# Performance work log

Measured on AMD Instinct MI355X. Metric: run time of the kernel, lower is better.

Reference implementation:

```python
import jax, jax.numpy as jnp
import numpy as np

EPS = 1e-5

def _layer_norm(x, w, b):
    mu = jnp.mean(x, axis=-1, keepdims=True)
    var = jnp.var(x, axis=-1, keepdims=True)
    return (x - mu) * jax.lax.rsqrt(var + EPS) * w + b

def setup_inputs() -> dict:
    key = jax.random.key(0)
    ks = jax.random.split(key, 9)
    B, N, D, H = 1, 768, 128, 128
    s_in = 1.0 / np.sqrt(D)
    s_h = 1.0 / np.sqrt(H)
    return {
        "x": jax.random.normal(ks[0], (B, N, N, D), dtype=jnp.float32),
        "mask": jnp.ones((B, N, N), dtype=jnp.float32),
        "norm_w": jnp.ones((D,), dtype=jnp.float32),
        "norm_b": jnp.zeros((D,), dtype=jnp.float32),
        "w_left": jax.random.normal(ks[1], (H, D), dtype=jnp.float32) * s_in,
        "w_right": jax.random.normal(ks[2], (H, D), dtype=jnp.float32) * s_in,
        "w_left_gate": jax.random.normal(ks[3], (H, D), dtype=jnp.float32) * s_in,
        "w_right_gate": jax.random.normal(ks[4], (H, D), dtype=jnp.float32) * s_in,
        "w_out_gate": jax.random.normal(ks[5], (H, D), dtype=jnp.float32) * s_in,
        "out_norm_w": jnp.ones((H,), dtype=jnp.float32),
        "out_norm_b": jnp.zeros((H,), dtype=jnp.float32),
        "w_out": jax.random.normal(ks[6], (D, H), dtype=jnp.float32) * s_h,
    }

def reference(x, mask, norm_w, norm_b, w_left, w_right, w_left_gate,
              w_right_gate, w_out_gate, out_norm_w, out_norm_b, w_out):
    # x: [B, N, N, D], mask: [B, N, N]
    xn = _layer_norm(x, norm_w, norm_b)
    m = mask[..., None]  # [B, N, N, 1]
    left = (xn @ w_left.T) * m * jax.nn.sigmoid(xn @ w_left_gate.T)
    right = (xn @ w_right.T) * m * jax.nn.sigmoid(xn @ w_right_gate.T)
    out_gate = jax.nn.sigmoid(xn @ w_out_gate.T)
    # per-channel triangular matmul in bf16, as in the original
    out = jnp.einsum('bikd,bjkd->bijd',
                     left.astype(jnp.bfloat16),
                     right.astype(jnp.bfloat16)).astype(jnp.float32)
    out = _layer_norm(out, out_norm_w, out_norm_b) * out_gate
    return out @ w_out.T
```

## Files before the change

kernel.cpp:

```cpp
#include <hip/hip_runtime.h>

typedef unsigned short u16;
typedef unsigned int   u32;
typedef short short8 __attribute__((ext_vector_type(8)));
typedef _Float16 half8 __attribute__((ext_vector_type(8)));
typedef float f32x4  __attribute__((ext_vector_type(4)));

#define NN 768
#define N2 (768*768)

__device__ __forceinline__ u16 f2b(float f) {
  u32 u = __float_as_uint(f);
  return (u16)((u + 0x7FFFu + ((u >> 16) & 1u)) >> 16);
}
__device__ __forceinline__ float b2f(u16 h) { return __uint_as_float(((u32)h) << 16); }
__device__ __forceinline__ u16 f2h(float f) {
  _Float16 h = (_Float16)f;
  return __builtin_bit_cast(u16, h);
}
__device__ __forceinline__ float h2f(u16 h) { return (float)__builtin_bit_cast(_Float16, h); }

__device__ __forceinline__ void gl_lds16(const void* g, void* lds) {
  __builtin_amdgcn_global_load_lds((__attribute__((address_space(1))) void*)(void*)g,
                                   (__attribute__((address_space(3))) void*)lds, 16, 0, 0);
}

__device__ __forceinline__ short8 frag256(const u16* base, int row, int k) {
  int c = k >> 3;
  int slot = ((c & 7) ^ (row & 7)) | (c & 8);
  return *(const short8*)(base + row*128 + slot*8);
}
__device__ __forceinline__ short8 frag128(const u16* base, int row, int k) {
  int c = k >> 3;
  int slot = (c ^ row) & 7;
  return *(const short8*)(base + row*64 + slot*8);
}
__device__ __forceinline__ f32x4 mfma_bf(short8 a, short8 b, f32x4 c) {
  return __builtin_amdgcn_mfma_f32_16x16x32_bf16(a, b, c, 0, 0, 0);
}
__device__ __forceinline__ f32x4 mfma_h(short8 a, short8 b, f32x4 c) {
  return __builtin_amdgcn_mfma_f32_16x16x32_f16(
      __builtin_bit_cast(half8, a), __builtin_bit_cast(half8, b), c, 0, 0, 0);
}

__global__ void k0_cvt(const float* __restrict__ w0, const float* __restrict__ w1,
                       const float* __restrict__ w2, const float* __restrict__ w3,
                       const float* __restrict__ w4, const float* __restrict__ w5,
                       u16* __restrict__ dst) {
  int idx = blockIdx.x*256 + threadIdx.x;
  int m = idx >> 14, o = idx & 16383;
  const float* s;
  switch (m) { case 0: s=w0; break; case 1: s=w1; break; case 2: s=w2; break;
               case 3: s=w3; break; case 4: s=w4; break; default: s=w5; }
  dst[idx] = f2h(s[o]);
}

__global__ __launch_bounds__(256, 2) void k1_proj(
    const float* __restrict__ x, const float* __restrict__ mask,
    const float* __restrict__ nw, const float* __restrict__ nb,
    const u16* __restrict__ wbf,
    u16* __restrict__ left_t, u16* __restrict__ right_t, u16* __restrict__ gate_ws)
{
  __shared__ __align__(16) u16 As[128*128];
  __shared__ __align__(16) u16 Bs[128*128];
  __shared__ float maskL[128];

  const int tid = threadIdx.x, w = tid>>6, l = tid&63;
  const long r0 = (long)blockIdx.x * 128;

  if (tid < 128) maskL[tid] = mask[r0 + tid];

  {
    const int c0v = l*2;
    const float nw0 = nw[c0v], nw1 = nw[c0v+1], nb0 = nb[c0v], nb1 = nb[c0v+1];
    for (int m = 0; m < 32; ++m) {
      int row = w*32 + m;
      float2 v = *(const float2*)(x + (r0 + row)*128 + c0v);
      float s = v.x + v.y, s2 = v.x*v.x + v.y*v.y;
      #pragma unroll
      for (int off = 1; off < 64; off <<= 1) {
        s  += __shfl_xor(s,  off, 64);
        s2 += __shfl_xor(s2, off, 64);
      }
      float mu = s * 0.0078125f;
      float rs = rsqrtf(s2 * 0.0078125f - mu*mu + 1e-5f);
      u32 pk = (u32)f2h((v.x - mu)*rs*nw0 + nb0)
             | ((u32)f2h((v.y - mu)*rs*nw1 + nb1) << 16);
      int c = l >> 2, slot = ((c&7)^(row&7)) | (c&8);
      *(u32*)(As + row*128 + slot*8 + (l&3)*2) = pk;
    }
  }
  __syncthreads();

  const int q = l>>4, mm = l&15;

  auto stageB = [&](const u16* wb) {
    #pragma unroll
    for (int c2 = 0; c2 < 8; ++c2) {
      int chunk = c2*4 + w;
      int rowv = chunk*4 + (l>>4);
      int sl = l & 15;
      int g16 = ((sl&7)^(rowv&7)) | (sl&8);
      gl_lds16(wb + rowv*128 + g16*8, Bs + chunk*512);
    }
  };

  f32x4 accA[2][8], accB[2][8];
  auto mfmaInto = [&](f32x4 (&acc)[2][8]) {
    #pragma unroll
    for (int rt = 0; rt < 2; ++rt)
      #pragma unroll
      for (int ct = 0; ct < 8; ++ct) acc[rt][ct] = (f32x4){0.f,0.f,0.f,0.f};
    #pragma unroll
    for (int ks = 0; ks < 4; ++ks) {
      int k = ks*32 + q*8;
      short8 a0 = frag256(As, w*32 + mm, k);
      short8 a1 = frag256(As, w*32 + 16 + mm, k);
      #pragma unroll
      for (int ct = 0; ct < 8; ++ct) {
        short8 bv = frag256(Bs, ct*16 + mm, k);
        acc[0][ct] = mfma_h(a0, bv, acc[0][ct]);
        acc[1][ct] = mfma_h(a1, bv, acc[1][ct]);
      }
    }
  };

  auto sigmoidAll = [&](f32x4 (&acc)[2][8]) {
    #pragma unroll
    for (int rt = 0; rt < 2; ++rt)
      #pragma unroll
      for (int ct = 0; ct < 8; ++ct)
        #pragma unroll
        for (int r = 0; r < 4; ++r)
          acc[rt][ct][r] = 1.f/(1.f + __expf(-acc[rt][ct][r]));
  };

  auto combineMask = [&](f32x4 (&av)[2][8], f32x4 (&ag)[2][8]) {
    float mk[2][4];
    #pragma unroll
    for (int rt = 0; rt < 2; ++rt)
      #pragma unroll
      for (int r = 0; r < 4; ++r) mk[rt][r] = maskL[w*32 + rt*16 + q*4 + r];
    #pragma unroll
    for (int rt = 0; rt < 2; ++rt)
      #pragma unroll
      for (int ct = 0; ct < 8; ++ct)
        #pragma unroll
        for (int r = 0; r < 4; ++r)
          av[rt][ct][r] *= mk[rt][r] * ag[rt][ct][r];
  };

  auto transposeStore = [&](f32x4 (&av)[2][8], u16* dst) {
    #pragma unroll
    for (int rt = 0; rt < 2; ++rt) {
      #pragma unroll
      for (int ct = 0; ct < 8; ++ct) {
        int kl = w*32 + rt*16 + q*4;
        int d  = ct*16 + mm;
        int c = kl >> 3, slot = ((c&7)^(d&7)) | (c&8);
        u32 p0 = (u32)f2b(av[rt][ct][0]) | ((u32)f2b(av[rt][ct][1])<<16);
        u32 p1 = (u32)f2b(av[rt][ct][2]) | ((u32)f2b(av[rt][ct][3])<<16);
        *(uint2*)(Bs + d*128 + slot*8 + (kl&7)) = make_uint2(p0, p1);
      }
    }
    __syncthreads();
    #pragma unroll
    for (int g = 0; g < 2; ++g) {
      int d = w*32 + g*16 + (l>>2);
      #pragma unroll
      for (int p = 0; p < 4; ++p) {
        int cc = p*4 + (l&3);
        int slot = ((cc&7)^(d&7)) | (cc&8);
        uint4 vv = *(const uint4*)(Bs + d*128 + slot*8);
        *(uint4*)(dst + (long)d*N2 + r0 + cc*8) = vv;
      }
    }
    __syncthreads();
  };

  stageB(wbf + 0*16384); __syncthreads();
  mfmaInto(accA); sigmoidAll(accA);
  __syncthreads();
  stageB(wbf + 1*16384); __syncthreads();
  mfmaInto(accB); combineMask(accB, accA);
  __syncthreads();
  transposeStore(accB, left_t);
  stageB(wbf + 2*16384); __syncthreads();
  mfmaInto(accA); sigmoidAll(accA);
  __syncthreads();
  stageB(wbf + 3*16384); __syncthreads();
  mfmaInto(accB); combineMask(accB, accA);
  __syncthreads();
  transposeStore(accB, right_t);
  stageB(wbf + 4*16384); __syncthreads();
  mfmaInto(accA); sigmoidAll(accA);
  #pragma unroll
  for (int rt = 0; rt < 2; ++rt)
    #pragma unroll
    for (int ct = 0; ct < 8; ++ct)
      #pragma unroll
      for (int r = 0; r < 4; ++r) {
        int row = w*32 + rt*16 + q*4 + r, dd = ct*16 + mm;
        gate_ws[(r0 + row)*128 + dd] = f2h(accA[rt][ct][r]);
      }
}

__global__ __launch_bounds__(256, 2) void k2_gemm(
    const u16* __restrict__ left_t, const u16* __restrict__ right_t, u16* __restrict__ out_ws)
{
  __shared__ __align__(16) u16 As[128*64];
  __shared__ __align__(16) u16 Bs[128*64];
  const int tid = threadIdx.x, w = tid>>6, l = tid&63;
  int bid = blockIdx.x;
  int d = bid / 36, t36 = bid % 36;
  int it = t36 / 6, jt = t36 % 6;
  const u16* Lb = left_t  + (long)d*N2 + (long)it*128*NN;
  const u16* Rb = right_t + (long)d*N2 + (long)jt*128*NN;
  const int wi = w & 1, wj = w >> 1;
  const int q = l>>4, mm = l&15;
  const int rloc = l>>3, sv = l&7;
  f32x4 acc[4][4];
  #pragma unroll
  for (int a2 = 0; a2 < 4; ++a2)
    #pragma unroll
    for (int b2 = 0; b2 < 4; ++b2) acc[a2][b2] = (f32x4){0.f,0.f,0.f,0.f};

  for (int kt = 0; kt < 12; ++kt) {
    __syncthreads();
    int k0 = kt*64;
    #pragma unroll
    for (int c2 = 0; c2 < 4; ++c2) {
      int chunk = c2*4 + w;
      int row = chunk*8 + rloc;
      int g8 = sv ^ (row & 7);
      gl_lds16(Lb + row*NN + k0 + g8*8, As + chunk*512);
      gl_lds16(Rb + row*NN + k0 + g8*8, Bs + chunk*512);
    }
    __syncthreads();
    #pragma unroll
    for (int kk = 0; kk < 64; kk += 32) {
      int k = kk + q*8;
      short8 af[4], bf[4];
      #pragma unroll
      for (int a2 = 0; a2 < 4; ++a2) af[a2] = frag128(As, wi*64 + a2*16 + mm, k);
      #pragma unroll
      for (int b2 = 0; b2 < 4; ++b2) bf[b2] = frag128(Bs, wj*64 + b2*16 + mm, k);
      #pragma unroll
      for (int a2 = 0; a2 < 4; ++a2)
        #pragma unroll
        for (int b2 = 0; b2 < 4; ++b2)
          acc[a2][b2] = mfma_bf(af[a2], bf[b2], acc[a2][b2]);
    }
  }
  u16* Ob = out_ws + (long)d*N2 + (long)(it*128)*NN + jt*128;
  #pragma unroll
  for (int a2 = 0; a2 < 4; ++a2)
    #pragma unroll
    for (int b2 = 0; b2 < 4; ++b2)
      #pragma unroll
      for (int r = 0; r < 4; ++r)
        Ob[(long)(wi*64 + a2*16 + q*4 + r)*NN + wj*64 + b2*16 + mm] = f2b(acc[a2][b2][r]);
}

__global__ __launch_bounds__(256, 2) void k3_out(
    const u16* __restrict__ out_ws, const u16* __restrict__ gate_ws,
    const float* __restrict__ onw, const float* __restrict__ onb,
    const u16* __restrict__ wbo, float* __restrict__ out)
{
  __shared__ __align__(16) u16 As[64*128];
  __shared__ __align__(16) u16 Bs[128*128];
  __shared__ float P[8][64];
  const int tid = threadIdx.x, w = tid>>6, l = tid&63;
  const int i = blockIdx.y, jt = blockIdx.x;
  const long base = (long)i*NN + jt*64;

  float v[32]; float s = 0.f, s2 = 0.f;
  const u16* src = out_ws + base + l;
  #pragma unroll
  for (int dd = 0; dd < 32; ++dd) {
    float f = b2f(src[(long)(w*32 + dd)*N2]);
    v[dd] = f; s += f; s2 += f*f;
  }
  P[w][l] = s; P[4+w][l] = s2;
  #pragma unroll
  for (int c2 = 0; c2 < 8; ++c2) {
    int chunk = c2*4 + w;
    int rowv = chunk*4 + (l>>4);
    int sl = l&15;
    int g16 = ((sl&7)^(rowv&7)) | (sl&8);
    gl_lds16(wbo + rowv*128 + g16*8, Bs + chunk*512);
  }
  __syncthreads();
  float sum = P[0][l]+P[1][l]+P[2][l]+P[3][l];
  float sq  = P[4][l]+P[5][l]+P[6][l]+P[7][l];
  float mu = sum * 0.0078125f;
  float rs = rsqrtf(sq * 0.0078125f - mu*mu + 1e-5f);

  const u16* gp = gate_ws + (base + l)*128 + w*32;
  #pragma unroll
  for (int hh = 0; hh < 32; hh += 2) {
    int h = w*32 + hh;
    u32 gpr = *(const u32*)(gp + hh);
    float g0 = h2f((u16)gpr), g1 = h2f((u16)(gpr>>16));
    float a0 = ((v[hh]   - mu)*rs*onw[h]   + onb[h])   * g0;
    float a1 = ((v[hh+1] - mu)*rs*onw[h+1] + onb[h+1]) * g1;
    u32 pk = (u32)f2h(a0) | ((u32)f2h(a1)<<16);
    int c = h >> 3, slot = ((c&7)^(l&7)) | (c&8);
    *(u32*)(As + l*128 + slot*8 + (h&7)) = pk;
  }
  __syncthreads();

  const int q = l>>4, mm = l&15;
  f32x4 acc[8];
  #pragma unroll
  for (int b2 = 0; b2 < 8; ++b2) acc[b2] = (f32x4){0.f,0.f,0.f,0.f};
  #pragma unroll
  for (int ks = 0; ks < 4; ++ks) {
    int k = ks*32 + q*8;
    short8 af = frag256(As, w*16 + mm, k);
    #pragma unroll
    for (int b2 = 0; b2 < 8; ++b2)
      acc[b2] = mfma_h(af, frag256(Bs, b2*16 + mm, k), acc[b2]);
  }
  float* ob = out + (base + w*16)*128;
  #pragma unroll
  for (int b2 = 0; b2 < 8; ++b2)
    #pragma unroll
    for (int r = 0; r < 4; ++r)
      ob[(long)(q*4 + r)*128 + b2*16 + mm] = acc[b2][r];
}

extern "C" void kernel_launch(void* const* d_in, const int* in_sizes, int n_in,
                              void* d_out, int out_size, void* d_ws, size_t ws_size,
                              hipStream_t stream) {
  const float* x    = (const float*)d_in[0];
  const float* mask = (const float*)d_in[1];
  const float* nw   = (const float*)d_in[2];
  const float* nb   = (const float*)d_in[3];
  const float* wl   = (const float*)d_in[4];
  const float* wr   = (const float*)d_in[5];
  const float* wlg  = (const float*)d_in[6];
  const float* wrg  = (const float*)d_in[7];
  const float* wog  = (const float*)d_in[8];
  const float* onw  = (const float*)d_in[9];
  const float* onb  = (const float*)d_in[10];
  const float* wo   = (const float*)d_in[11];

  if (ws_size < (size_t)4*N2*128*2 + 6*16384*2) return;
  u16* left_t  = (u16*)d_ws;
  u16* right_t = left_t  + (size_t)N2*128;
  u16* gate_ws = right_t + (size_t)N2*128;
  u16* out_ws  = gate_ws + (size_t)N2*128;
  u16* wbf     = out_ws  + (size_t)N2*128;

  k0_cvt<<<384, 256, 0, stream>>>(wlg, wl, wrg, wr, wog, wo, wbf);
  k1_proj<<<4608, 256, 0, stream>>>(x, mask, nw, nb, wbf, left_t, right_t, gate_ws);
  k2_gemm<<<4608, 256, 0, stream>>>(left_t, right_t, out_ws);
  k3_out<<<dim3(12, 768), 256, 0, stream>>>(out_ws, gate_ws, onw, onb, wbf + 5*16384, (float*)d_out);
}
```

Before: 1.138 ms.

## Restructure projection kernel: global-fragment weights, fused gate pairs, transposed gate layout

```diff
diff --git a/kernel.cpp b/kernel.cpp
--- a/kernel.cpp
+++ b/kernel.cpp
@@ -35,34 +35,47 @@
   int slot = (c ^ row) & 7;
   return *(const short8*)(base + row*64 + slot*8);
 }
+__device__ __forceinline__ short8 fragG(const u16* wg, int row, int k) {
+  return *(const short8*)(wg + (((k >> 3)*128) + row)*8);
+}
 __device__ __forceinline__ f32x4 mfma_bf(short8 a, short8 b, f32x4 c) {
   return __builtin_amdgcn_mfma_f32_16x16x32_bf16(a, b, c, 0, 0, 0);
 }
 __device__ __forceinline__ f32x4 mfma_h(short8 a, short8 b, f32x4 c) {
   return __builtin_amdgcn_mfma_f32_16x16x32_f16(
       __builtin_bit_cast(half8, a), __builtin_bit_cast(half8, b), c, 0, 0, 0);
+}
+__device__ __forceinline__ float sigm(float x) {
+  return __builtin_amdgcn_rcpf(1.f + __expf(-x));
 }
 
 __global__ void k0_cvt(const float* __restrict__ w0, const float* __restrict__ w1,
                        const float* __restrict__ w2, const float* __restrict__ w3,
                        const float* __restrict__ w4, const float* __restrict__ w5,
                        u16* __restrict__ dst) {
-  int idx = blockIdx.x*256 + threadIdx.x;
-  int m = idx >> 14, o = idx & 16383;
+  int t = blockIdx.x*256 + threadIdx.x;
+  int m = t >> 11, o = t & 2047;
+  int h = o >> 4, c = o & 15;
   const float* s;
   switch (m) { case 0: s=w0; break; case 1: s=w1; break; case 2: s=w2; break;
                case 3: s=w3; break; case 4: s=w4; break; default: s=w5; }
-  dst[idx] = f2h(s[o]);
+  const float* p = s + h*128 + c*8;
+  float4 f0 = *(const float4*)p;
+  float4 f1 = *(const float4*)(p + 4);
+  short8 r;
+  r[0]=(short)f2h(f0.x); r[1]=(short)f2h(f0.y); r[2]=(short)f2h(f0.z); r[3]=(short)f2h(f0.w);
+  r[4]=(short)f2h(f1.x); r[5]=(short)f2h(f1.y); r[6]=(short)f2h(f1.z); r[7]=(short)f2h(f1.w);
+  *(short8*)(dst + (size_t)m*16384 + (size_t)(c*128 + h)*8) = r;
 }
 
 __global__ __launch_bounds__(256, 2) void k1_proj(
     const float* __restrict__ x, const float* __restrict__ mask,
     const float* __restrict__ nw, const float* __restrict__ nb,
     const u16* __restrict__ wbf,
-    u16* __restrict__ left_t, u16* __restrict__ right_t, u16* __restrict__ gate_ws)
+    u16* __restrict__ left_t, u16* __restrict__ right_t, u16* __restrict__ gate_t)
 {
   __shared__ __align__(16) u16 As[128*128];
-  __shared__ __align__(16) u16 Bs[128*128];
+  __shared__ __align__(16) u16 Ts[128*128];
   __shared__ float maskL[128];
 
   const int tid = threadIdx.x, w = tid>>6, l = tid&63;
@@ -71,138 +84,132 @@
   if (tid < 128) maskL[tid] = mask[r0 + tid];
 
   {
-    const int c0v = l*2;
-    const float nw0 = nw[c0v], nw1 = nw[c0v+1], nb0 = nb[c0v], nb1 = nb[c0v+1];
-    for (int m = 0; m < 32; ++m) {
-      int row = w*32 + m;
-      float2 v = *(const float2*)(x + (r0 + row)*128 + c0v);
-      float s = v.x + v.y, s2 = v.x*v.x + v.y*v.y;
-      #pragma unroll
-      for (int off = 1; off < 64; off <<= 1) {
+    const int g = l >> 4, sl = l & 15;
+    const float4 nw0 = *(const float4*)(nw + sl*8);
+    const float4 nw1 = *(const float4*)(nw + sl*8 + 4);
+    const float4 nb0 = *(const float4*)(nb + sl*8);
+    const float4 nb1 = *(const float4*)(nb + sl*8 + 4);
+    #pragma unroll
+    for (int it = 0; it < 8; ++it) {
+      int row = w*32 + it*4 + g;
+      const float* xp = x + (r0 + row)*128 + sl*8;
+      float4 v0 = *(const float4*)xp;
+      float4 v1 = *(const float4*)(xp + 4);
+      float s  = (v0.x+v0.y) + (v0.z+v0.w) + (v1.x+v1.y) + (v1.z+v1.w);
+      float s2 = (v0.x*v0.x+v0.y*v0.y) + (v0.z*v0.z+v0.w*v0.w)
+               + (v1.x*v1.x+v1.y*v1.y) + (v1.z*v1.z+v1.w*v1.w);
+      #pragma unroll
+      for (int off = 1; off < 16; off <<= 1) {
         s  += __shfl_xor(s,  off, 64);
         s2 += __shfl_xor(s2, off, 64);
       }
       float mu = s * 0.0078125f;
-      float rs = rsqrtf(s2 * 0.0078125f - mu*mu + 1e-5f);
-      u32 pk = (u32)f2h((v.x - mu)*rs*nw0 + nb0)
-             | ((u32)f2h((v.y - mu)*rs*nw1 + nb1) << 16);
-      int c = l >> 2, slot = ((c&7)^(row&7)) | (c&8);
-      *(u32*)(As + row*128 + slot*8 + (l&3)*2) = pk;
+      float rs = __builtin_amdgcn_rsqf(s2 * 0.0078125f - mu*mu + 1e-5f);
+      short8 rr;
+      rr[0] = (short)f2h((v0.x-mu)*rs*nw0.x + nb0.x);
+      rr[1] = (short)f2h((v0.y-mu)*rs*nw0.y + nb0.y);
+      rr[2] = (short)f2h((v0.z-mu)*rs*nw0.z + nb0.z);
+      rr[3] = (short)f2h((v0.w-mu)*rs*nw0.w + nb0.w);
+      rr[4] = (short)f2h((v1.x-mu)*rs*nw1.x + nb1.x);
+      rr[5] = (short)f2h((v1.y-mu)*rs*nw1.y + nb1.y);
+      rr[6] = (short)f2h((v1.z-mu)*rs*nw1.z + nb1.z);
+      rr[7] = (short)f2h((v1.w-mu)*rs*nw1.w + nb1.w);
+      int slot = ((sl&7)^(row&7)) | (sl&8);
+      *(short8*)(As + row*128 + slot*8) = rr;
     }
   }
   __syncthreads();
 
   const int q = l>>4, mm = l&15;
-
-  auto stageB = [&](const u16* wb) {
-    #pragma unroll
-    for (int c2 = 0; c2 < 8; ++c2) {
-      int chunk = c2*4 + w;
-      int rowv = chunk*4 + (l>>4);
-      int sl = l & 15;
-      int g16 = ((sl&7)^(rowv&7)) | (sl&8);
-      gl_lds16(wb + rowv*128 + g16*8, Bs + chunk*512);
-    }
-  };
-
-  f32x4 accA[2][8], accB[2][8];
-  auto mfmaInto = [&](f32x4 (&acc)[2][8]) {
-    #pragma unroll
-    for (int rt = 0; rt < 2; ++rt)
-      #pragma unroll
-      for (int ct = 0; ct < 8; ++ct) acc[rt][ct] = (f32x4){0.f,0.f,0.f,0.f};
+  const int wi = w & 1, wj = w >> 1;
+
+  float mk[4][4];
+  #pragma unroll
+  for (int a2 = 0; a2 < 4; ++a2)
+    #pragma unroll
+    for (int r = 0; r < 4; ++r)
+      mk[a2][r] = maskL[wi*64 + a2*16 + q*4 + r];
+
+  auto pairPass = [&](const u16* wG, const u16* wM, bool hasMain, bool fp16out, u16* dst) {
+    f32x4 accG[4][4], accM[4][4];
+    #pragma unroll
+    for (int a2 = 0; a2 < 4; ++a2)
+      #pragma unroll
+      for (int b2 = 0; b2 < 4; ++b2) {
+        accG[a2][b2] = (f32x4){0.f,0.f,0.f,0.f};
+        accM[a2][b2] = (f32x4){0.f,0.f,0.f,0.f};
+      }
     #pragma unroll
     for (int ks = 0; ks < 4; ++ks) {
       int k = ks*32 + q*8;
-      short8 a0 = frag256(As, w*32 + mm, k);
-      short8 a1 = frag256(As, w*32 + 16 + mm, k);
-      #pragma unroll
-      for (int ct = 0; ct < 8; ++ct) {
-        short8 bv = frag256(Bs, ct*16 + mm, k);
-        acc[0][ct] = mfma_h(a0, bv, acc[0][ct]);
-        acc[1][ct] = mfma_h(a1, bv, acc[1][ct]);
-      }
-    }
-  };
-
-  auto sigmoidAll = [&](f32x4 (&acc)[2][8]) {
-    #pragma unroll
-    for (int rt = 0; rt < 2; ++rt)
-      #pragma unroll
-      for (int ct = 0; ct < 8; ++ct)
+      short8 a[4];
+      #pragma unroll
+      for (int a2 = 0; a2 < 4; ++a2) a[a2] = frag256(As, wi*64 + a2*16 + mm, k);
+      #pragma unroll
+      for (int b2 = 0; b2 < 4; ++b2) {
+        short8 bg = fragG(wG, wj*64 + b2*16 + mm, k);
+        #pragma unroll
+        for (int a2 = 0; a2 < 4; ++a2) accG[a2][b2] = mfma_h(a[a2], bg, accG[a2][b2]);
+        if (hasMain) {
+          short8 bm = fragG(wM, wj*64 + b2*16 + mm, k);
+          #pragma unroll
+          for (int a2 = 0; a2 < 4; ++a2) accM[a2][b2] = mfma_h(a[a2], bm, accM[a2][b2]);
+        }
+      }
+    }
+    #pragma unroll
+    for (int a2 = 0; a2 < 4; ++a2)
+      #pragma unroll
+      for (int b2 = 0; b2 < 4; ++b2)
         #pragma unroll
         for (int r = 0; r < 4; ++r)
-          acc[rt][ct][r] = 1.f/(1.f + __expf(-acc[rt][ct][r]));
-  };
-
-  auto combineMask = [&](f32x4 (&av)[2][8], f32x4 (&ag)[2][8]) {
-    float mk[2][4];
-    #pragma unroll
-    for (int rt = 0; rt < 2; ++rt)
-      #pragma unroll
-      for (int r = 0; r < 4; ++r) mk[rt][r] = maskL[w*32 + rt*16 + q*4 + r];
-    #pragma unroll
-    for (int rt = 0; rt < 2; ++rt)
-      #pragma unroll
-      for (int ct = 0; ct < 8; ++ct)
+          accG[a2][b2][r] = sigm(accG[a2][b2][r]);
+    if (hasMain) {
+      #pragma unroll
+      for (int a2 = 0; a2 < 4; ++a2)
         #pragma unroll
-        for (int r = 0; r < 4; ++r)
-          av[rt][ct][r] *= mk[rt][r] * ag[rt][ct][r];
-  };
-
-  auto transposeStore = [&](f32x4 (&av)[2][8], u16* dst) {
-    #pragma unroll
-    for (int rt = 0; rt < 2; ++rt) {
-      #pragma unroll
-      for (int ct = 0; ct < 8; ++ct) {
-        int kl = w*32 + rt*16 + q*4;
-        int d  = ct*16 + mm;
+        for (int b2 = 0; b2 < 4; ++b2)
+          #pragma unroll
+          for (int r = 0; r < 4; ++r)
+            accM[a2][b2][r] *= mk[a2][r] * accG[a2][b2][r];
+    }
+    f32x4 (*res)[4] = hasMain ? accM : accG;
+    #pragma unroll
+    for (int a2 = 0; a2 < 4; ++a2)
+      #pragma unroll
+      for (int b2 = 0; b2 < 4; ++b2) {
+        int kl = wi*64 + a2*16 + q*4;
+        int d  = wj*64 + b2*16 + mm;
         int c = kl >> 3, slot = ((c&7)^(d&7)) | (c&8);
-        u32 p0 = (u32)f2b(av[rt][ct][0]) | ((u32)f2b(av[rt][ct][1])<<16);
-        u32 p1 = (u32)f2b(av[rt][ct][2]) | ((u32)f2b(av[rt][ct][3])<<16);
-        *(uint2*)(Bs + d*128 + slot*8 + (kl&7)) = make_uint2(p0, p1);
-      }
-    }
+        f32x4 t = res[a2][b2];
+        u32 p0, p1;
+        if (fp16out) {
+          p0 = (u32)f2h(t[0]) | ((u32)f2h(t[1])<<16);
+          p1 = (u32)f2h(t[2]) | ((u32)f2h(t[3])<<16);
+        } else {
+          p0 = (u32)f2b(t[0]) | ((u32)f2b(t[1])<<16);
+          p1 = (u32)f2b(t[2]) | ((u32)f2b(t[3])<<16);
+        }
+        *(uint2*)(Ts + d*128 + slot*8 + (kl&7)) = make_uint2(p0, p1);
+      }
     __syncthreads();
     #pragma unroll
-    for (int g = 0; g < 2; ++g) {
-      int d = w*32 + g*16 + (l>>2);
+    for (int g2 = 0; g2 < 2; ++g2) {
+      int d = w*32 + g2*16 + (l>>2);
       #pragma unroll
       for (int p = 0; p < 4; ++p) {
         int cc = p*4 + (l&3);
         int slot = ((cc&7)^(d&7)) | (cc&8);
-        uint4 vv = *(const uint4*)(Bs + d*128 + slot*8);
+        uint4 vv = *(const uint4*)(Ts + d*128 + slot*8);
         *(uint4*)(dst + (long)d*N2 + r0 + cc*8) = vv;
       }
     }
     __syncthreads();
   };
 
-  stageB(wbf + 0*16384); __syncthreads();
-  mfmaInto(accA); sigmoidAll(accA);
-  __syncthreads();
-  stageB(wbf + 1*16384); __syncthreads();
-  mfmaInto(accB); combineMask(accB, accA);
-  __syncthreads();
-  transposeStore(accB, left_t);
-  stageB(wbf + 2*16384); __syncthreads();
-  mfmaInto(accA); sigmoidAll(accA);
-  __syncthreads();
-  stageB(wbf + 3*16384); __syncthreads();
-  mfmaInto(accB); combineMask(accB, accA);
-  __syncthreads();
-  transposeStore(accB, right_t);
-  stageB(wbf + 4*16384); __syncthreads();
-  mfmaInto(accA); sigmoidAll(accA);
-  #pragma unroll
-  for (int rt = 0; rt < 2; ++rt)
-    #pragma unroll
-    for (int ct = 0; ct < 8; ++ct)
-      #pragma unroll
-      for (int r = 0; r < 4; ++r) {
-        int row = w*32 + rt*16 + q*4 + r, dd = ct*16 + mm;
-        gate_ws[(r0 + row)*128 + dd] = f2h(accA[rt][ct][r]);
-      }
+  pairPass(wbf + 0*16384, wbf + 1*16384, true,  false, left_t);
+  pairPass(wbf + 2*16384, wbf + 3*16384, true,  false, right_t);
+  pairPass(wbf + 4*16384, wbf + 4*16384, false, true,  gate_t);
 }
 
 __global__ __launch_bounds__(256, 2) void k2_gemm(
@@ -211,7 +218,8 @@
   __shared__ __align__(16) u16 As[128*64];
   __shared__ __align__(16) u16 Bs[128*64];
   const int tid = threadIdx.x, w = tid>>6, l = tid&63;
-  int bid = blockIdx.x;
+  int bid0 = blockIdx.x;
+  int bid = (bid0 & 7)*576 + (bid0 >> 3);
   int d = bid / 36, t36 = bid % 36;
   int it = t36 / 6, jt = t36 % 6;
   const u16* Lb = left_t  + (long)d*N2 + (long)it*128*NN;
@@ -262,13 +270,12 @@
         Ob[(long)(wi*64 + a2*16 + q*4 + r)*NN + wj*64 + b2*16 + mm] = f2b(acc[a2][b2][r]);
 }
 
-__global__ __launch_bounds__(256, 2) void k3_out(
-    const u16* __restrict__ out_ws, const u16* __restrict__ gate_ws,
+__global__ __launch_bounds__(256, 4) void k3_out(
+    const u16* __restrict__ out_ws, const u16* __restrict__ gate_t,
     const float* __restrict__ onw, const float* __restrict__ onb,
     const u16* __restrict__ wbo, float* __restrict__ out)
 {
   __shared__ __align__(16) u16 As[64*128];
-  __shared__ __align__(16) u16 Bs[128*128];
   __shared__ float P[8][64];
   const int tid = threadIdx.x, w = tid>>6, l = tid&63;
   const int i = blockIdx.y, jt = blockIdx.x;
@@ -282,26 +289,18 @@
     v[dd] = f; s += f; s2 += f*f;
   }
   P[w][l] = s; P[4+w][l] = s2;
-  #pragma unroll
-  for (int c2 = 0; c2 < 8; ++c2) {
-    int chunk = c2*4 + w;
-    int rowv = chunk*4 + (l>>4);
-    int sl = l&15;
-    int g16 = ((sl&7)^(rowv&7)) | (sl&8);
-    gl_lds16(wbo + rowv*128 + g16*8, Bs + chunk*512);
-  }
   __syncthreads();
   float sum = P[0][l]+P[1][l]+P[2][l]+P[3][l];
   float sq  = P[4][l]+P[5][l]+P[6][l]+P[7][l];
   float mu = sum * 0.0078125f;
-  float rs = rsqrtf(sq * 0.0078125f - mu*mu + 1e-5f);
-
-  const u16* gp = gate_ws + (base + l)*128 + w*32;
+  float rs = __builtin_amdgcn_rsqf(sq * 0.0078125f - mu*mu + 1e-5f);
+
+  const u16* gp = gate_t + base + l;
   #pragma unroll
   for (int hh = 0; hh < 32; hh += 2) {
     int h = w*32 + hh;
-    u32 gpr = *(const u32*)(gp + hh);
-    float g0 = h2f((u16)gpr), g1 = h2f((u16)(gpr>>16));
+    float g0 = h2f(gp[(long)h*N2]);
+    float g1 = h2f(gp[(long)(h+1)*N2]);
     float a0 = ((v[hh]   - mu)*rs*onw[h]   + onb[h])   * g0;
     float a1 = ((v[hh+1] - mu)*rs*onw[h+1] + onb[h+1]) * g1;
     u32 pk = (u32)f2h(a0) | ((u32)f2h(a1)<<16);
@@ -320,7 +319,7 @@
     short8 af = frag256(As, w*16 + mm, k);
     #pragma unroll
     for (int b2 = 0; b2 < 8; ++b2)
-      acc[b2] = mfma_h(af, frag256(Bs, b2*16 + mm, k), acc[b2]);
+      acc[b2] = mfma_h(af, fragG(wbo, b2*16 + mm, k), acc[b2]);
   }
   float* ob = out + (base + w*16)*128;
   #pragma unroll
@@ -349,12 +348,12 @@
   if (ws_size < (size_t)4*N2*128*2 + 6*16384*2) return;
   u16* left_t  = (u16*)d_ws;
   u16* right_t = left_t  + (size_t)N2*128;
-  u16* gate_ws = right_t + (size_t)N2*128;
-  u16* out_ws  = gate_ws + (size_t)N2*128;
+  u16* gate_t  = right_t + (size_t)N2*128;
+  u16* out_ws  = gate_t  + (size_t)N2*128;
   u16* wbf     = out_ws  + (size_t)N2*128;
 
-  k0_cvt<<<384, 256, 0, stream>>>(wlg, wl, wrg, wr, wog, wo, wbf);
-  k1_proj<<<4608, 256, 0, stream>>>(x, mask, nw, nb, wbf, left_t, right_t, gate_ws);
+  k0_cvt<<<48, 256, 0, stream>>>(wlg, wl, wrg, wr, wog, wo, wbf);
+  k1_proj<<<4608, 256, 0, stream>>>(x, mask, nw, nb, wbf, left_t, right_t, gate_t);
   k2_gemm<<<4608, 256, 0, stream>>>(left_t, right_t, out_ws);
-  k3_out<<<dim3(12, 768), 256, 0, stream>>>(out_ws, gate_ws, onw, onb, wbf + 5*16384, (float*)d_out);
-}
+  k3_out<<<dim3(12, 768), 256, 0, stream>>>(out_ws, gate_t, onw, onb, wbf + 5*16384, (float*)d_out);
+}
```

New measurement: 955.5 us. -16.1%, faster.
